# Kernel tuning notes

Measured on AMD Instinct MI355X. Metric: run time of the kernel, lower is better.

## Reference

```python
import jax, jax.numpy as jnp
import numpy as np

IN_F, HID, OUT, NN = 64, 128, 64, 128
TOTAL = 4096  # 32 graphs * 128 nodes


def setup_inputs() -> dict:
    key = jax.random.key(0)
    ks = jax.random.split(key, 8)
    d_in = 1 + 2 * IN_F
    s1 = 1.0 / np.sqrt(d_in)
    s2 = 1.0 / np.sqrt(HID)
    return {
        "feat": jax.random.normal(ks[0], (TOTAL, IN_F), jnp.float32),
        "coordinate": jax.random.normal(ks[1], (TOTAL, 3), jnp.float32),
        "W1": jax.random.uniform(ks[2], (d_in, HID), jnp.float32, -s1, s1),
        "b1": jax.random.uniform(ks[3], (HID,), jnp.float32, -s1, s1),
        "W2": jax.random.uniform(ks[4], (HID, HID), jnp.float32, -s2, s2),
        "b2": jax.random.uniform(ks[5], (HID,), jnp.float32, -s2, s2),
        "W3": jax.random.uniform(ks[6], (HID, OUT), jnp.float32, -s2, s2),
        "b3": jax.random.uniform(ks[7], (OUT,), jnp.float32, -s2, s2),
        "num_nodes": NN,
    }


def reference(feat, coordinate, W1, b1, W2, b2, W3, b3, num_nodes):
    N = num_nodes
    B = feat.shape[0] // N
    h = feat.reshape(B, N, -1)        # [B,N,F]
    x = coordinate.reshape(B, N, -1)  # [B,N,3]
    # pairwise squared distance: [B,N,N,1]
    d2 = jnp.sum((x[:, None, :, :] - x[:, :, None, :]) ** 2, axis=-1, keepdims=True)
    F = h.shape[-1]
    # feat concat order matches torch: [h_j broadcast over dim1, h_i broadcast over dim2]
    hj = jnp.broadcast_to(h[:, None, :, :], (B, N, N, F))
    hi = jnp.broadcast_to(h[:, :, None, :], (B, N, N, F))
    z = jnp.concatenate([d2, hj, hi], axis=-1)  # [B,N,N,1+2F]
    z = jax.nn.silu(z @ W1 + b1)
    z = jax.nn.silu(z @ W2 + b2)
    z = z @ W3 + b3                   # [B,N,N,OUT]
    return jnp.sum(z, axis=(1, 2))    # [B,OUT]
```

## Files before the change

### kernel.cpp

```cpp
#include <hip/hip_runtime.h>
#include <hip/hip_bf16.h>

#define F_IN 64
#define HID 128
#define OUTF 64
#define NN 128
#define NB 32
#define TOTAL 4096

#define NEG_LOG2E (-1.4426950408889634f)
#define NEG_LN2 (-0.6931471805599453f)

typedef short bf16x8 __attribute__((ext_vector_type(8)));
typedef float f32x4 __attribute__((ext_vector_type(4)));

static __device__ __forceinline__ short f2bf(float v) {
  __hip_bfloat16 h = __float2bfloat16(v);
  return __builtin_bit_cast(short, h);
}

static __device__ __forceinline__ float fexp2(float x) {
#if __has_builtin(__builtin_amdgcn_exp2f)
  return __builtin_amdgcn_exp2f(x);
#else
  return exp2f(x);
#endif
}

__global__ __launch_bounds__(256) void uv_prep(
    const float* __restrict__ feat,
    const float* __restrict__ W1,
    const float* __restrict__ W2,
    const float* __restrict__ b1,
    const float* __restrict__ b2,
    float* __restrict__ uvp,
    __hip_bfloat16* __restrict__ w2swz,
    float* __restrict__ w0p,
    float* __restrict__ b2p) {
  __shared__ __align__(16) char wcat[256 * 128];
  const int tid = threadIdx.x;
  {
    const int c = tid;
    const int cc = c & 127;
    const int rbase = (c < HID) ? 1 : 65;
#pragma unroll
    for (int p = 0; p < 8; ++p) {
      bf16x8 pk;
#pragma unroll
      for (int m = 0; m < 8; ++m)
        pk[m] = f2bf(W1[(rbase + p * 8 + m) * HID + cc]);
      *reinterpret_cast<bf16x8*>(wcat + c * 128 + ((p ^ (c & 7)) << 4)) = pk;
    }
  }
  if (blockIdx.x < 64) {
    const int e = blockIdx.x * 256 + tid;
    const int kk = e >> 7, cc2 = e & 127;
    const int byo = cc2 * 256 + (((kk >> 3) ^ (cc2 & 7)) << 4) + (kk & 7) * 2;
    *reinterpret_cast<__hip_bfloat16*>(reinterpret_cast<char*>(w2swz) + byo) =
        __float2bfloat16(W2[kk * HID + cc2]);
  } else if (blockIdx.x == 64) {
    if (tid < HID) w0p[tid] = NEG_LOG2E * W1[tid];
    else b2p[tid - HID] = NEG_LOG2E * b2[tid - HID];
  }
  __syncthreads();

  const int wave = tid >> 6, lane = tid & 63;
  const int lr = lane & 15, kg = lane >> 4;
  const int r0 = blockIdx.x * 16;

  f32x4 acc[4];
#pragma unroll
  for (int ct = 0; ct < 4; ++ct) acc[ct] = {0.f, 0.f, 0.f, 0.f};

#pragma unroll
  for (int ks = 0; ks < 2; ++ks) {
    const float* fp = feat + (size_t)(r0 + lr) * F_IN + ks * 32 + kg * 8;
    const f32x4 fa = *reinterpret_cast<const f32x4*>(fp);
    const f32x4 fb = *reinterpret_cast<const f32x4*>(fp + 4);
    bf16x8 a;
#pragma unroll
    for (int m = 0; m < 4; ++m) {
      a[m] = f2bf(fa[m]);
      a[4 + m] = f2bf(fb[m]);
    }
    const int slot = ks * 4 + kg;
#pragma unroll
    for (int ct = 0; ct < 4; ++ct) {
      const int c = wave * 64 + ct * 16 + lr;
      const bf16x8 w = *reinterpret_cast<const bf16x8*>(
          wcat + c * 128 + ((slot ^ (c & 7)) << 4));
      acc[ct] = __builtin_amdgcn_mfma_f32_16x16x32_bf16(a, w, acc[ct], 0, 0, 0);
    }
  }
#pragma unroll
  for (int ct = 0; ct < 4; ++ct) {
    const int c = wave * 64 + ct * 16 + lr;
    const float badd = (c >= HID) ? b1[c - HID] : 0.f;
#pragma unroll
    for (int reg = 0; reg < 4; ++reg) {
      const int r = r0 + kg * 4 + reg;
      uvp[(size_t)r * 256 + c] = NEG_LOG2E * (acc[ct][reg] + badd);
    }
  }
}

__global__ __launch_bounds__(256, 4) void sake_main(
    const float* __restrict__ coord,
    const float* __restrict__ w0p,
    const float* __restrict__ b2p,
    const float* __restrict__ uvp,
    const __hip_bfloat16* __restrict__ w2swz,
    float* __restrict__ part) {
  __shared__ __align__(16) char w2lds[HID * 256];
  __shared__ float ssum[4][HID];

  const int tid = threadIdx.x;
  const int bid = (blockIdx.x & 7) * 512 + (blockIdx.x >> 3);
  const int b = bid >> 7, i = bid & 127;

  {
    const char* src = reinterpret_cast<const char*>(w2swz);
#pragma unroll
    for (int p = 0; p < 8; ++p) {
      const int o = tid * 16 + p * 4096;
      *reinterpret_cast<int4*>(w2lds + o) =
          *reinterpret_cast<const int4*>(src + o);
    }
  }

  const int wave = tid >> 6, lane = tid & 63;
  const int lr = lane & 15, kg = lane >> 4;
  const int j0 = wave * 32;

  const float* xi = coord + (size_t)(b * NN + i) * 3;
  const float xix = xi[0], xiy = xi[1], xiz = xi[2];
  float d2t[2];
#pragma unroll
  for (int t = 0; t < 2; ++t) {
    const float* xj = coord + (size_t)(b * NN + j0 + t * 16 + lr) * 3;
    const float dx = xj[0] - xix, dy = xj[1] - xiy, dz = xj[2] - xiz;
    d2t[t] = dx * dx + dy * dy + dz * dz;
  }

  f32x4 acc[2][8];
#pragma unroll
  for (int c = 0; c < 8; ++c) {
    const float bb = b2p[c * 16 + lr];
    acc[0][c] = {bb, bb, bb, bb};
    acc[1][c] = {bb, bb, bb, bb};
  }

  const float* vrow = uvp + ((size_t)b * NN + i) * 256 + HID;
  const float* u0 = uvp + ((size_t)b * NN + j0 + lr) * 256;
  const float* u1 = u0 + 16 * 256;

  __syncthreads();

#pragma unroll
  for (int ks = 0; ks < 4; ++ks) {
    const int c0 = ks * 32 + kg * 8;
    bf16x8 zb[2];
#pragma unroll
    for (int t = 0; t < 2; ++t) {
      const float* up = (t ? u1 : u0) + c0;
#pragma unroll
      for (int h = 0; h < 2; ++h) {
        const f32x4 u4 = *reinterpret_cast<const f32x4*>(up + h * 4);
        const f32x4 v4 = *reinterpret_cast<const f32x4*>(vrow + c0 + h * 4);
        const f32x4 w4 = *reinterpret_cast<const f32x4*>(w0p + c0 + h * 4);
#pragma unroll
        for (int m = 0; m < 4; ++m) {
          const float z = fmaf(d2t[t], w4[m], u4[m] + v4[m]);
          zb[t][h * 4 + m] = f2bf(z * __builtin_amdgcn_rcpf(1.f + fexp2(z)));
        }
      }
    }
    const int rbase = lr * 256 + ((((ks << 2) | kg) ^ (lr & 7)) << 4);
    bf16x8 wf[4];
#pragma unroll
    for (int c = 0; c < 4; ++c)
      wf[c] = *reinterpret_cast<const bf16x8*>(w2lds + rbase + c * 4096);
#pragma unroll
    for (int c = 0; c < 4; ++c) {
      acc[0][c] = __builtin_amdgcn_mfma_f32_16x16x32_bf16(zb[0], wf[c], acc[0][c], 0, 0, 0);
      acc[1][c] = __builtin_amdgcn_mfma_f32_16x16x32_bf16(zb[1], wf[c], acc[1][c], 0, 0, 0);
    }
#pragma unroll
    for (int c = 0; c < 4; ++c)
      wf[c] = *reinterpret_cast<const bf16x8*>(w2lds + rbase + (4 + c) * 4096);
#pragma unroll
    for (int c = 0; c < 4; ++c) {
      acc[0][4 + c] = __builtin_amdgcn_mfma_f32_16x16x32_bf16(zb[0], wf[c], acc[0][4 + c], 0, 0, 0);
      acc[1][4 + c] = __builtin_amdgcn_mfma_f32_16x16x32_bf16(zb[1], wf[c], acc[1][4 + c], 0, 0, 0);
    }
  }

#pragma unroll
  for (int c = 0; c < 8; ++c) {
    float s = 0.f;
#pragma unroll
    for (int t = 0; t < 2; ++t)
#pragma unroll
      for (int m = 0; m < 4; ++m) {
        const float z = acc[t][c][m];
        s = fmaf(z, __builtin_amdgcn_rcpf(1.f + fexp2(z)), s);
      }
    s += __shfl_xor(s, 16);
    s += __shfl_xor(s, 32);
    acc[0][c][0] = s;
  }
  if (lane < 16) {
#pragma unroll
    for (int c = 0; c < 8; ++c) ssum[wave][c * 16 + lane] = acc[0][c][0];
  }
  __syncthreads();
  if (tid < HID) {
    part[(size_t)bid * HID + tid] =
        ssum[0][tid] + ssum[1][tid] + ssum[2][tid] + ssum[3][tid];
  }
}

__global__ void final_kernel(const float* __restrict__ part,
                             const float* __restrict__ W3,
                             const float* __restrict__ b3,
                             float* __restrict__ out) {
  __shared__ float s2[2][HID];
  __shared__ float s[HID];
  int b = blockIdx.x, t = threadIdx.x;
  int c = t & 127, half = t >> 7;
  float a = 0.f;
  for (int g = half * 64; g < half * 64 + 64; ++g)
    a += part[(size_t)(b * NN + g) * HID + c];
  s2[half][c] = a;
  __syncthreads();
  if (t < HID) s[t] = (s2[0][t] + s2[1][t]) * NEG_LN2;
  __syncthreads();
  if (t < OUTF) {
    float o = 16384.f * b3[t];
    for (int c2 = 0; c2 < HID; ++c2) o += s[c2] * W3[c2 * OUTF + t];
    out[b * OUTF + t] = o;
  }
}

extern "C" void kernel_launch(void* const* d_in, const int* in_sizes, int n_in,
                              void* d_out, int out_size, void* d_ws, size_t ws_size,
                              hipStream_t stream) {
  const float* feat = (const float*)d_in[0];
  const float* coord = (const float*)d_in[1];
  const float* W1 = (const float*)d_in[2];
  const float* b1 = (const float*)d_in[3];
  const float* W2 = (const float*)d_in[4];
  const float* b2 = (const float*)d_in[5];
  const float* W3 = (const float*)d_in[6];
  const float* b3 = (const float*)d_in[7];
  float* out = (float*)d_out;

  char* ws = (char*)d_ws;
  __hip_bfloat16* w2swz = (__hip_bfloat16*)ws;
  float* w0p = (float*)(ws + 32 * 1024);
  float* b2p = (float*)(ws + 36 * 1024);
  float* uvp = (float*)(ws + 64 * 1024);
  float* part = (float*)(ws + 64 * 1024 + 4096 * 1024);

  uv_prep<<<256, 256, 0, stream>>>(feat, W1, W2, b1, b2, uvp, w2swz, w0p, b2p);
  sake_main<<<TOTAL, 256, 0, stream>>>(coord, w0p, b2p, uvp, w2swz, part);
  final_kernel<<<NB, 256, 0, stream>>>(part, W3, b3, out);
}
```

Measured before the change: 60.48 us.

## Process eight i-rows per block to amortize W2 LDS staging across rows

The main kernel now launches 512 blocks of 512 threads. Each block handles one graph's group of 8 i-rows, with 8 waves covering the 128 j nodes, instead of one block per (b,i) pair. The 32 KB W2 copy into LDS and the per-thread u-row and coordinate loads are paid once per 8 rows rather than once per row. The per-row silu outputs are accumulated in registers, and the partial buffer and final reduction shrink to 16 entries per graph. In exchange there are fewer blocks (512 across the GPU), a serial 8-iteration loop per block, and each wave holds only one 16-row MFMA tile, so there is less independent work to hide latency.

```diff
diff --git a/kernel.cpp b/kernel.cpp
--- a/kernel.cpp
+++ b/kernel.cpp
@@ -104,7 +104,7 @@
   }
 }
 
-__global__ __launch_bounds__(256, 4) void sake_main(
+__global__ __launch_bounds__(512, 4) void sake_main(
     const float* __restrict__ coord,
     const float* __restrict__ w0p,
     const float* __restrict__ b2p,
@@ -112,17 +112,18 @@
     const __hip_bfloat16* __restrict__ w2swz,
     float* __restrict__ part) {
   __shared__ __align__(16) char w2lds[HID * 256];
-  __shared__ float ssum[4][HID];
+  __shared__ float ssum[8][HID];
 
   const int tid = threadIdx.x;
-  const int bid = (blockIdx.x & 7) * 512 + (blockIdx.x >> 3);
-  const int b = bid >> 7, i = bid & 127;
+  const int bid = (blockIdx.x & 7) * 64 + (blockIdx.x >> 3);
+  const int b = bid >> 4;
+  const int ig = bid & 15;
 
   {
     const char* src = reinterpret_cast<const char*>(w2swz);
 #pragma unroll
-    for (int p = 0; p < 8; ++p) {
-      const int o = tid * 16 + p * 4096;
+    for (int p = 0; p < 4; ++p) {
+      const int o = tid * 16 + p * 8192;
       *reinterpret_cast<int4*>(w2lds + o) =
           *reinterpret_cast<const int4*>(src + o);
     }
@@ -130,93 +131,98 @@
 
   const int wave = tid >> 6, lane = tid & 63;
   const int lr = lane & 15, kg = lane >> 4;
-  const int j0 = wave * 32;
-
-  const float* xi = coord + (size_t)(b * NN + i) * 3;
-  const float xix = xi[0], xiy = xi[1], xiz = xi[2];
-  float d2t[2];
-#pragma unroll
-  for (int t = 0; t < 2; ++t) {
-    const float* xj = coord + (size_t)(b * NN + j0 + t * 16 + lr) * 3;
-    const float dx = xj[0] - xix, dy = xj[1] - xiy, dz = xj[2] - xiz;
-    d2t[t] = dx * dx + dy * dy + dz * dz;
-  }
-
-  f32x4 acc[2][8];
+  const int j = wave * 16 + lr;
+
+  const float* urow = uvp + ((size_t)b * NN + j) * 256;
+  const float* xjp = coord + (size_t)(b * NN + j) * 3;
+  const float xjx = xjp[0], xjy = xjp[1], xjz = xjp[2];
+
+  float bb[8];
+#pragma unroll
+  for (int c = 0; c < 8; ++c) bb[c] = b2p[c * 16 + lr];
+
+  float csum[8];
+#pragma unroll
+  for (int c = 0; c < 8; ++c) csum[c] = 0.f;
+
+  __syncthreads();
+
+#pragma unroll 1
+  for (int it = 0; it < 8; ++it) {
+    const int i = ig * 8 + it;
+    const float* xip = coord + (size_t)(b * NN + i) * 3;
+    const float dx = xjx - xip[0], dy = xjy - xip[1], dz = xjz - xip[2];
+    const float d2 = dx * dx + dy * dy + dz * dz;
+    const float* vrow = uvp + ((size_t)b * NN + i) * 256 + HID;
+
+    f32x4 acc[8];
+#pragma unroll
+    for (int c = 0; c < 8; ++c) acc[c] = {bb[c], bb[c], bb[c], bb[c]};
+
+#pragma unroll
+    for (int ks = 0; ks < 4; ++ks) {
+      const int c0 = ks * 32 + kg * 8;
+      const f32x4 u0 = *reinterpret_cast<const f32x4*>(urow + c0);
+      const f32x4 u1 = *reinterpret_cast<const f32x4*>(urow + c0 + 4);
+      const f32x4 v0 = *reinterpret_cast<const f32x4*>(vrow + c0);
+      const f32x4 v1 = *reinterpret_cast<const f32x4*>(vrow + c0 + 4);
+      const f32x4 w0 = *reinterpret_cast<const f32x4*>(w0p + c0);
+      const f32x4 w1 = *reinterpret_cast<const f32x4*>(w0p + c0 + 4);
+
+      bf16x8 zb;
+#pragma unroll
+      for (int m = 0; m < 4; ++m) {
+        const float z = fmaf(d2, w0[m], u0[m] + v0[m]);
+        zb[m] = f2bf(z * __builtin_amdgcn_rcpf(1.f + fexp2(z)));
+      }
+#pragma unroll
+      for (int m = 0; m < 4; ++m) {
+        const float z = fmaf(d2, w1[m], u1[m] + v1[m]);
+        zb[4 + m] = f2bf(z * __builtin_amdgcn_rcpf(1.f + fexp2(z)));
+      }
+
+      const int rbase = lr * 256 + ((((ks << 2) | kg) ^ (lr & 7)) << 4);
+      bf16x8 wf[4];
+#pragma unroll
+      for (int c = 0; c < 4; ++c)
+        wf[c] = *reinterpret_cast<const bf16x8*>(w2lds + rbase + c * 4096);
+#pragma unroll
+      for (int c = 0; c < 4; ++c)
+        acc[c] = __builtin_amdgcn_mfma_f32_16x16x32_bf16(zb, wf[c], acc[c], 0, 0, 0);
+#pragma unroll
+      for (int c = 0; c < 4; ++c)
+        wf[c] = *reinterpret_cast<const bf16x8*>(w2lds + rbase + (4 + c) * 4096);
+#pragma unroll
+      for (int c = 0; c < 4; ++c)
+        acc[4 + c] = __builtin_amdgcn_mfma_f32_16x16x32_bf16(zb, wf[c], acc[4 + c], 0, 0, 0);
+    }
+
+#pragma unroll
+    for (int c = 0; c < 8; ++c)
+#pragma unroll
+      for (int m = 0; m < 4; ++m) {
+        const float z = acc[c][m];
+        csum[c] = fmaf(z, __builtin_amdgcn_rcpf(1.f + fexp2(z)), csum[c]);
+      }
+  }
+
 #pragma unroll
   for (int c = 0; c < 8; ++c) {
-    const float bb = b2p[c * 16 + lr];
-    acc[0][c] = {bb, bb, bb, bb};
-    acc[1][c] = {bb, bb, bb, bb};
-  }
-
-  const float* vrow = uvp + ((size_t)b * NN + i) * 256 + HID;
-  const float* u0 = uvp + ((size_t)b * NN + j0 + lr) * 256;
-  const float* u1 = u0 + 16 * 256;
-
-  __syncthreads();
-
-#pragma unroll
-  for (int ks = 0; ks < 4; ++ks) {
-    const int c0 = ks * 32 + kg * 8;
-    bf16x8 zb[2];
-#pragma unroll
-    for (int t = 0; t < 2; ++t) {
-      const float* up = (t ? u1 : u0) + c0;
-#pragma unroll
-      for (int h = 0; h < 2; ++h) {
-        const f32x4 u4 = *reinterpret_cast<const f32x4*>(up + h * 4);
-        const f32x4 v4 = *reinterpret_cast<const f32x4*>(vrow + c0 + h * 4);
-        const f32x4 w4 = *reinterpret_cast<const f32x4*>(w0p + c0 + h * 4);
-#pragma unroll
-        for (int m = 0; m < 4; ++m) {
-          const float z = fmaf(d2t[t], w4[m], u4[m] + v4[m]);
-          zb[t][h * 4 + m] = f2bf(z * __builtin_amdgcn_rcpf(1.f + fexp2(z)));
-        }
-      }
-    }
-    const int rbase = lr * 256 + ((((ks << 2) | kg) ^ (lr & 7)) << 4);
-    bf16x8 wf[4];
-#pragma unroll
-    for (int c = 0; c < 4; ++c)
-      wf[c] = *reinterpret_cast<const bf16x8*>(w2lds + rbase + c * 4096);
-#pragma unroll
-    for (int c = 0; c < 4; ++c) {
-      acc[0][c] = __builtin_amdgcn_mfma_f32_16x16x32_bf16(zb[0], wf[c], acc[0][c], 0, 0, 0);
-      acc[1][c] = __builtin_amdgcn_mfma_f32_16x16x32_bf16(zb[1], wf[c], acc[1][c], 0, 0, 0);
-    }
-#pragma unroll
-    for (int c = 0; c < 4; ++c)
-      wf[c] = *reinterpret_cast<const bf16x8*>(w2lds + rbase + (4 + c) * 4096);
-#pragma unroll
-    for (int c = 0; c < 4; ++c) {
-      acc[0][4 + c] = __builtin_amdgcn_mfma_f32_16x16x32_bf16(zb[0], wf[c], acc[0][4 + c], 0, 0, 0);
-      acc[1][4 + c] = __builtin_amdgcn_mfma_f32_16x16x32_bf16(zb[1], wf[c], acc[1][4 + c], 0, 0, 0);
-    }
-  }
-
-#pragma unroll
-  for (int c = 0; c < 8; ++c) {
-    float s = 0.f;
-#pragma unroll
-    for (int t = 0; t < 2; ++t)
-#pragma unroll
-      for (int m = 0; m < 4; ++m) {
-        const float z = acc[t][c][m];
-        s = fmaf(z, __builtin_amdgcn_rcpf(1.f + fexp2(z)), s);
-      }
+    float s = csum[c];
     s += __shfl_xor(s, 16);
     s += __shfl_xor(s, 32);
-    acc[0][c][0] = s;
+    csum[c] = s;
   }
   if (lane < 16) {
 #pragma unroll
-    for (int c = 0; c < 8; ++c) ssum[wave][c * 16 + lane] = acc[0][c][0];
+    for (int c = 0; c < 8; ++c) ssum[wave][c * 16 + lane] = csum[c];
   }
   __syncthreads();
   if (tid < HID) {
-    part[(size_t)bid * HID + tid] =
-        ssum[0][tid] + ssum[1][tid] + ssum[2][tid] + ssum[3][tid];
+    float s = 0.f;
+#pragma unroll
+    for (int w = 0; w < 8; ++w) s += ssum[w][tid];
+    part[(size_t)bid * HID + tid] = s;
   }
 }
 
@@ -229,8 +235,8 @@
   int b = blockIdx.x, t = threadIdx.x;
   int c = t & 127, half = t >> 7;
   float a = 0.f;
-  for (int g = half * 64; g < half * 64 + 64; ++g)
-    a += part[(size_t)(b * NN + g) * HID + c];
+  for (int g = half * 8; g < half * 8 + 8; ++g)
+    a += part[(size_t)(b * 16 + g) * HID + c];
   s2[half][c] = a;
   __syncthreads();
   if (t < HID) s[t] = (s2[0][t] + s2[1][t]) * NEG_LN2;
@@ -263,6 +269,6 @@
   float* part = (float*)(ws + 64 * 1024 + 4096 * 1024);
 
   uv_prep<<<256, 256, 0, stream>>>(feat, W1, W2, b1, b2, uvp, w2swz, w0p, b2p);
-  sake_main<<<TOTAL, 256, 0, stream>>>(coord, w0p, b2p, uvp, w2swz, part);
+  sake_main<<<512, 512, 0, stream>>>(coord, w0p, b2p, uvp, w2swz, part);
   final_kernel<<<NB, 256, 0, stream>>>(part, W3, b3, out);
 }
```

Result: slower. 231.3 us (+282.5%).
